# Optimization experiments

Hardware: AMD Instinct MI355X
Metric: run time of the kernel (lower is better)

## Reference

```python
import jax, jax.numpy as jnp
import numpy as np
import math

BASE_RES = 16; SCALE = 1.47; N_LEVELS = 16; FDIM = 2; MAX_SPLASH = 4
LOG2 = 17; HM = 1 << LOG2; SPLITS = [0.9375, 0.875]  # sorted descending as in module


def _build_cfg():
    res = [int(BASE_RES * SCALE ** i) for i in range(N_LEVELS)]
    ns = [0] * N_LEVELS
    for i in range(N_LEVELS):
        for j, s in enumerate(SPLITS):
            if i >= N_LEVELS * s:
                ns[i] = MAX_SPLASH // (2 ** j)
                break
    nidx = [min(r ** 3, HM) for r in res]
    nfeat = [nidx[i] * max(ns[i], 1) for i in range(N_LEVELS)]
    ngau = [nidx[i] * ns[i] for i in range(N_LEVELS)]
    fb = np.concatenate([[0], np.cumsum(nfeat)]).astype(np.int64)
    gb = np.concatenate([[0], np.cumsum(ngau)]).astype(np.int64)
    return res, ns, nidx, fb, gb

RES, NS, NIDX, FB, GB = _build_cfg()
OFFS = np.array([[(k >> 2) & 1, (k >> 1) & 1, k & 1] for k in range(8)], dtype=np.int32)
PRIMES = np.array([1, 2654435761, 805459861], dtype=np.uint32)
SQRT2PI = math.sqrt(2.0 * math.pi)


def _corners_coeffs(coords, res):
    # coords: (N,3) in [0,1). Returns corners (N,8,3) int32 and trilinear coeffs (N,8).
    x = jnp.clip(res * coords, 0.0, res - 1.001)
    pos = jnp.floor(x).astype(jnp.int32)
    xf = x - pos.astype(coords.dtype)
    offs = jnp.asarray(OFFS)
    corners = pos[:, None, :] + offs[None]
    w = jnp.where(offs[None].astype(bool), xf[:, None, :], 1.0 - xf[:, None, :])
    return corners, jnp.prod(w, axis=-1)


def _hash_index(corners, res):
    # linear index if grid fits in table, else xor-prime spatial hash (mod 2^17)
    if res ** 3 <= HM:
        return corners[..., 0] + corners[..., 1] * res + corners[..., 2] * (res * res)
    c = corners.astype(jnp.uint32)
    p = jnp.asarray(PRIMES)
    h = (c[..., 0] * p[0]) ^ (c[..., 1] * p[1]) ^ (c[..., 2] * p[2])
    return (h & jnp.uint32(HM - 1)).astype(jnp.int32)


def setup_inputs() -> dict:
    key = jax.random.key(0)
    k1, k2, k3, k4 = jax.random.split(key, 4)
    N = 262144
    coords = jax.random.uniform(k1, (N, 3), dtype=jnp.float32)
    feats = 0.01 * jax.random.normal(k2, (int(FB[-1]), FDIM), dtype=jnp.float32)
    # means: uniform in a ball of radius 0.25 centered at 0.5 (init_mean)
    G = int(GB[-1])
    pts = jax.random.normal(k3, (G, 3), dtype=jnp.float32)
    r = jnp.sqrt(jax.random.uniform(jax.random.fold_in(k3, 1), (G, 1), dtype=jnp.float32))
    means = pts / jnp.linalg.norm(pts, axis=1, keepdims=True) * r * 0.25 + 0.5
    # stds: N(0.125, 0.02) as in fixed_std=False branch
    stds = 0.125 + 0.02 * jax.random.normal(k4, (G, 1), dtype=jnp.float32)
    return {"coords": coords, "feats": feats, "means": means, "stds": stds}


def reference(coords, feats, means, stds):
    out_feats = []
    out_gmm = []
    for i in range(N_LEVELS):
        res = RES[i]; ns = NS[i]
        corners, coeffs = _corners_coeffs(coords, res)  # (N,8,3), (N,8)
        idx = _hash_index(corners, res)                 # (N,8)
        f = feats[int(FB[i]):int(FB[i + 1])].reshape(-1, max(ns, 1), FDIM)[idx]  # (N,8,S,F)
        if ns:
            m = means[int(GB[i]):int(GB[i + 1])].reshape(-1, ns, 3)[idx]   # (N,8,S,3)
            s = jnp.abs(stds[int(GB[i]):int(GB[i + 1])].reshape(-1, ns, 1)[idx])  # (N,8,S,1)
            diff = coords[:, None, None, :] - m
            sq = jnp.sum(diff * diff / (2.0 * s * s + 1e-7), axis=-1, keepdims=True)
            gw = jnp.exp(-sq) / (SQRT2PI * s + 1e-7)                        # Gaussian weights
            dw = jnp.sum(jnp.abs(diff / s) ** 2, axis=-1, keepdims=True)    # normalized sq dist
            out_feats.append(jnp.einsum('nc,ncsf->nf', coeffs, gw * f))
            out_gmm.append(jnp.einsum('nc,ncs->n', coeffs, (gw * dw)[..., 0]))
        else:
            out_feats.append(jnp.einsum('nc,ncf->nf', coeffs, f[:, :, 0, :]))
    return jnp.concatenate(out_feats, axis=-1), jnp.stack(out_gmm, axis=-1)
```

## Files before the change

kernel.cpp:

```cpp
#include <hip/hip_runtime.h>
#include <math.h>


#define HMASK 131071
typedef float vf4 __attribute__((ext_vector_type(4)));
typedef _Float16 h8 __attribute__((ext_vector_type(8)));
typedef _Float16 h2 __attribute__((ext_vector_type(2)));

__constant__ int c_fbh[10] = {180567,311639,442711,573783,704855,835927,
                              966999,1098071,1229143,1360215};

__device__ __forceinline__ void corner_setup(int res, float cx, float cy, float cz,
                                             int& px, int& py, int& pz,
                                             float& fx, float& fy, float& fz)
{
    const float hi = (float)((double)res - 1.001);
    float x = fminf(fmaxf((float)res * cx, 0.0f), hi);
    float y = fminf(fmaxf((float)res * cy, 0.0f), hi);
    float z = fminf(fmaxf((float)res * cz, 0.0f), hi);
    px = (int)x; py = (int)y; pz = (int)z;
    fx = x - (float)px; fy = y - (float)py; fz = z - (float)pz;
}

template<bool HASH>
__device__ __forceinline__ float2 plain_eval(
    int res, int fbase, float cx, float cy, float cz,
    const float* __restrict__ feats)
{
    int px, py, pz; float fx, fy, fz;
    corner_setup(res, cx, cy, cz, px, py, pz, fx, fy, fz);
    int   idxs[8];
    float ws[8];
#pragma unroll
    for (int k = 0; k < 8; ++k) {
        const int ox = (k >> 2) & 1, oy = (k >> 1) & 1, oz = k & 1;
        const int ix = px + ox, iy = py + oy, iz = pz + oz;
        ws[k] = (ox ? fx : 1.0f - fx) * (oy ? fy : 1.0f - fy) * (oz ? fz : 1.0f - fz);
        if (HASH) {
            unsigned h = (unsigned)ix ^ ((unsigned)iy * 2654435761u) ^ ((unsigned)iz * 805459861u);
            idxs[k] = (int)(h & HMASK);
        } else {
            idxs[k] = ix + iy * res + iz * res * res;
        }
    }
    float2 fv[8];
#pragma unroll
    for (int k = 0; k < 8; ++k)
        fv[k] = *(const float2*)(feats + (size_t)(fbase + idxs[k]) * 2);
    float a0 = 0.0f, a1 = 0.0f;
#pragma unroll
    for (int k = 0; k < 8; ++k) { a0 += ws[k] * fv[k].x; a1 += ws[k] * fv[k].y; }
    return make_float2(a0, a1);
}

__device__ __forceinline__ float2 plain_eval_h(
    int res, const h2* __restrict__ tab, float cx, float cy, float cz)
{
    int px, py, pz; float fx, fy, fz;
    corner_setup(res, cx, cy, cz, px, py, pz, fx, fy, fz);
    int   idxs[8];
    float ws[8];
#pragma unroll
    for (int k = 0; k < 8; ++k) {
        const int ox = (k >> 2) & 1, oy = (k >> 1) & 1, oz = k & 1;
        const int ix = px + ox, iy = py + oy, iz = pz + oz;
        ws[k] = (ox ? fx : 1.0f - fx) * (oy ? fy : 1.0f - fy) * (oz ? fz : 1.0f - fz);
        unsigned h = (unsigned)ix ^ ((unsigned)iy * 2654435761u) ^ ((unsigned)iz * 805459861u);
        idxs[k] = (int)(h & HMASK);
    }
    h2 fv[8];
#pragma unroll
    for (int k = 0; k < 8; ++k) fv[k] = tab[idxs[k]];
    float a0 = 0.0f, a1 = 0.0f;
#pragma unroll
    for (int k = 0; k < 8; ++k) { a0 += ws[k] * (float)fv[k][0]; a1 += ws[k] * (float)fv[k][1]; }
    return make_float2(a0, a1);
}

__device__ __forceinline__ void gauss_pre(float w, float dx, float dy, float dz,
                                          float i2s, float inrm, float is2,
                                          float f0, float f1,
                                          float& a0, float& a1, float& ag)
{
    const float d2 = dx*dx + dy*dy + dz*dz;
    const float sq = d2 * i2s;
    const float gw = __expf(-sq) * inrm;
    const float wg = w * gw;
    a0 += wg * f0;
    a1 += wg * f1;
    ag += wg * (d2 * is2);
}

__device__ __forceinline__ void splash14_part(
    int k0, float cx, float cy, float cz, float cox, float coy, float coz,
    const h8* __restrict__ slots, float& a0, float& a1, float& ag)
{
    int px, py, pz; float fx, fy, fz;
    corner_setup(3520, cx, cy, cz, px, py, pz, fx, fy, fz);
    a0 = 0.0f; a1 = 0.0f; ag = 0.0f;
#pragma unroll
    for (int kk = 0; kk < 4; ++kk) {
        const int k = k0 + kk;
        const int ox = (k >> 2) & 1, oy = (k >> 1) & 1, oz = k & 1;
        const int ix = px + ox, iy = py + oy, iz = pz + oz;
        const float w = (ox ? fx : 1.0f - fx) * (oy ? fy : 1.0f - fy) * (oz ? fz : 1.0f - fz);
        unsigned h = (unsigned)ix ^ ((unsigned)iy * 2654435761u) ^ ((unsigned)iz * 805459861u);
        const int idx = (int)(h & HMASK);
        const h8* sp = slots + (size_t)idx * 2;
        h8 A = sp[0], B = sp[1];
        gauss_pre(w, cox - (float)A[0], coy - (float)A[1], coz - (float)A[2],
                  (float)A[6], (float)B[0], (float)B[2], (float)B[4], (float)B[5], a0, a1, ag);
        gauss_pre(w, cox - (float)A[3], coy - (float)A[4], coz - (float)A[5],
                  (float)A[7], (float)B[1], (float)B[3], (float)B[6], (float)B[7], a0, a1, ag);
    }
}

__device__ __forceinline__ void splash15_part(
    int k0, float cx, float cy, float cz, float cox, float coy, float coz,
    const h8* __restrict__ slots, float& a0, float& a1, float& ag)
{
    int px, py, pz; float fx, fy, fz;
    corner_setup(5174, cx, cy, cz, px, py, pz, fx, fy, fz);
    a0 = 0.0f; a1 = 0.0f; ag = 0.0f;
#pragma unroll
    for (int kk = 0; kk < 2; ++kk) {
        const int k = k0 + kk;
        const int ox = (k >> 2) & 1, oy = (k >> 1) & 1, oz = k & 1;
        const int ix = px + ox, iy = py + oy, iz = pz + oz;
        const float w = (ox ? fx : 1.0f - fx) * (oy ? fy : 1.0f - fy) * (oz ? fz : 1.0f - fz);
        unsigned h = (unsigned)ix ^ ((unsigned)iy * 2654435761u) ^ ((unsigned)iz * 805459861u);
        const int idx = (int)(h & HMASK);
        const h8* sp = slots + (size_t)idx * 4;
        h8 A = sp[0], B = sp[1], C = sp[2], D = sp[3];
        gauss_pre(w, cox - (float)A[0], coy - (float)A[1], coz - (float)A[2],
                  (float)B[4], (float)C[0], (float)C[4], (float)D[0], (float)D[1], a0, a1, ag);
        gauss_pre(w, cox - (float)A[3], coy - (float)A[4], coz - (float)A[5],
                  (float)B[5], (float)C[1], (float)C[5], (float)D[2], (float)D[3], a0, a1, ag);
        gauss_pre(w, cox - (float)A[6], coy - (float)A[7], coz - (float)B[0],
                  (float)B[6], (float)C[2], (float)C[6], (float)D[4], (float)D[5], a0, a1, ag);
        gauss_pre(w, cox - (float)B[1], coy - (float)B[2], coz - (float)B[3],
                  (float)B[7], (float)C[3], (float)C[7], (float)D[6], (float)D[7], a0, a1, ag);
    }
}

template<int NS, int KN>
__device__ __forceinline__ void splash_direct_part(
    int k0, int res, int fbase, int gbase, float cx, float cy, float cz,
    const float* __restrict__ feats, const float* __restrict__ means,
    const float* __restrict__ stds, float& a0, float& a1, float& ag)
{
    int px, py, pz; float fx, fy, fz;
    corner_setup(res, cx, cy, cz, px, py, pz, fx, fy, fz);
    a0 = 0.0f; a1 = 0.0f; ag = 0.0f;
#pragma unroll
    for (int kk = 0; kk < KN; ++kk) {
        const int k = k0 + kk;
        const int ox = (k >> 2) & 1, oy = (k >> 1) & 1, oz = k & 1;
        const int ix = px + ox, iy = py + oy, iz = pz + oz;
        const float w = (ox ? fx : 1.0f - fx) * (oy ? fy : 1.0f - fy) * (oz ? fz : 1.0f - fz);
        unsigned h = (unsigned)ix ^ ((unsigned)iy * 2654435761u) ^ ((unsigned)iz * 805459861u);
        const int idx = (int)(h & HMASK);
        const int grow = gbase + idx * NS;
        const float* m = means + (size_t)grow * 3;
        const float* s = stds + grow;
        const float* f = feats + (size_t)(fbase + idx * NS) * 2;
#pragma unroll
        for (int si = 0; si < NS; ++si) {
            const float dx = cx - m[3*si], dy = cy - m[3*si+1], dz = cz - m[3*si+2];
            const float sva = fabsf(s[si]);
            const float d2 = dx*dx + dy*dy + dz*dz;
            const float s2 = sva * sva;
            const float sq = d2 / (2.0f * s2 + 1e-7f);
            const float gw = expf(-sq) / (2.5066282746310002f * sva + 1e-7f);
            const float wg = w * gw;
            a0 += wg * f[2*si];
            a1 += wg * f[2*si+1];
            ag += wg * (d2 / s2);
        }
    }
}

__global__ __launch_bounds__(256) void repack_kernel(
    const float* __restrict__ means, const float* __restrict__ stds,
    const float* __restrict__ feats, _Float16* __restrict__ ws)
{
    const int i = blockIdx.x * 256 + threadIdx.x;
    if (i < 1310720) {
        const int lvl = i >> 17;
        const int e   = i & 131071;
        const float2 f = *(const float2*)(feats + (size_t)(c_fbh[lvl] + e) * 2);
        h2 v; v[0] = (_Float16)f.x; v[1] = (_Float16)f.y;
        ((h2*)ws)[lvl * 131072 + e] = v;
    } else if (i < 1441792) {
        const int e = i - 1310720;
        const float2* m2 = (const float2*)(means + (size_t)e * 6);
        const float2 ma = m2[0], mb = m2[1], mc = m2[2];
        const float2 sv = *(const float2*)(stds + 2 * e);
        const float2* f2 = (const float2*)(feats + (size_t)(1491287 + 2 * e) * 2);
        const float2 fa = f2[0], fb = f2[1];
        const float s0 = fabsf(sv.x), s1 = fabsf(sv.y);
        h8 A, B;
        A[0] = (_Float16)(ma.x - 0.5f); A[1] = (_Float16)(ma.y - 0.5f); A[2] = (_Float16)(mb.x - 0.5f);
        A[3] = (_Float16)(mb.y - 0.5f); A[4] = (_Float16)(mc.x - 0.5f); A[5] = (_Float16)(mc.y - 0.5f);
        A[6] = (_Float16)(1.0f / (2.0f * s0 * s0 + 1e-7f));
        A[7] = (_Float16)(1.0f / (2.0f * s1 * s1 + 1e-7f));
        B[0] = (_Float16)(1.0f / (2.5066282746310002f * s0 + 1e-7f));
        B[1] = (_Float16)(1.0f / (2.5066282746310002f * s1 + 1e-7f));
        B[2] = (_Float16)(1.0f / (s0 * s0));
        B[3] = (_Float16)(1.0f / (s1 * s1));
        B[4] = (_Float16)fa.x; B[5] = (_Float16)fa.y; B[6] = (_Float16)fb.x; B[7] = (_Float16)fb.y;
        h8* dst = (h8*)(ws + 2621440) + (size_t)e * 2;
        dst[0] = A; dst[1] = B;
    } else {
        const int e = i - 1441792;
        const vf4* m4 = (const vf4*)(means + (size_t)(262144 + 4 * e) * 3);
        const vf4 u = m4[0], v = m4[1], w = m4[2];
        const vf4 s4 = *(const vf4*)(stds + 262144 + 4 * e);
        const float2* f2 = (const float2*)(feats + (size_t)(1753431 + 4 * e) * 2);
        const float2 fa = f2[0], fb = f2[1], fc = f2[2], fd = f2[3];
        h8 A, B, C, D;
        A[0] = (_Float16)(u.x - 0.5f); A[1] = (_Float16)(u.y - 0.5f); A[2] = (_Float16)(u.z - 0.5f);
        A[3] = (_Float16)(u.w - 0.5f); A[4] = (_Float16)(v.x - 0.5f); A[5] = (_Float16)(v.y - 0.5f);
        A[6] = (_Float16)(v.z - 0.5f); A[7] = (_Float16)(v.w - 0.5f);
        B[0] = (_Float16)(w.x - 0.5f); B[1] = (_Float16)(w.y - 0.5f);
        B[2] = (_Float16)(w.z - 0.5f); B[3] = (_Float16)(w.w - 0.5f);
        const float sv[4] = {fabsf(s4.x), fabsf(s4.y), fabsf(s4.z), fabsf(s4.w)};
#pragma unroll
        for (int t = 0; t < 4; ++t) {
            B[4 + t] = (_Float16)(1.0f / (2.0f * sv[t] * sv[t] + 1e-7f));
            C[t]     = (_Float16)(1.0f / (2.5066282746310002f * sv[t] + 1e-7f));
            C[4 + t] = (_Float16)(1.0f / (sv[t] * sv[t]));
        }
        D[0] = (_Float16)fa.x; D[1] = (_Float16)fa.y; D[2] = (_Float16)fb.x; D[3] = (_Float16)fb.y;
        D[4] = (_Float16)fc.x; D[5] = (_Float16)fc.y; D[6] = (_Float16)fd.x; D[7] = (_Float16)fd.y;
        h8* dst = (h8*)(ws + 4718592) + (size_t)e * 4;
        dst[0] = A; dst[1] = B; dst[2] = C; dst[3] = D;
    }
}

template<bool PACKED>
__global__ __launch_bounds__(256) void splash_enc(
    const float* __restrict__ coords, const float* __restrict__ feats,
    const float* __restrict__ means,  const float* __restrict__ stds,
    const _Float16* __restrict__ ws, float* __restrict__ out, int N)
{
    const int b = blockIdx.x;
    const int tid = threadIdx.x;
    const h2* tabs = (const h2*)ws;
    float* gmm = out + (size_t)N * 32;

    if (b < 1024) {
        const int n = b * 256 + tid;
        const float cx = coords[3*n+0], cy = coords[3*n+1], cz = coords[3*n+2];
        float2 acc[8];
        acc[0] = plain_eval<false>(16,       0, cx, cy, cz, feats);
        acc[1] = plain_eval<false>(23,    4096, cx, cy, cz, feats);
        acc[2] = plain_eval<false>(34,   16263, cx, cy, cz, feats);
        acc[3] = plain_eval<false>(50,   55567, cx, cy, cz, feats);
        if (PACKED) {
            acc[4] = plain_eval_h(74,  tabs + 0 * 131072, cx, cy, cz);
            acc[5] = plain_eval_h(109, tabs + 1 * 131072, cx, cy, cz);
            acc[6] = plain_eval_h(161, tabs + 2 * 131072, cx, cy, cz);
            acc[7] = plain_eval_h(237, tabs + 3 * 131072, cx, cy, cz);
        } else {
            acc[4] = plain_eval<true>(74,  180567, cx, cy, cz, feats);
            acc[5] = plain_eval<true>(109, 311639, cx, cy, cz, feats);
            acc[6] = plain_eval<true>(161, 442711, cx, cy, cz, feats);
            acc[7] = plain_eval<true>(237, 573783, cx, cy, cz, feats);
        }
        vf4* o = (vf4*)(out + (size_t)n * 32);
        o[0] = (vf4){acc[0].x, acc[0].y, acc[1].x, acc[1].y};
        o[1] = (vf4){acc[2].x, acc[2].y, acc[3].x, acc[3].y};
        o[2] = (vf4){acc[4].x, acc[4].y, acc[5].x, acc[5].y};
        o[3] = (vf4){acc[6].x, acc[6].y, acc[7].x, acc[7].y};
    } else if (b < 2048) {
        const int n = (b - 1024) * 256 + tid;
        const float cx = coords[3*n+0], cy = coords[3*n+1], cz = coords[3*n+2];
        float2 acc[6];
        if (PACKED) {
            acc[0] = plain_eval_h(348,  tabs + 4 * 131072, cx, cy, cz);
            acc[1] = plain_eval_h(512,  tabs + 5 * 131072, cx, cy, cz);
            acc[2] = plain_eval_h(753,  tabs + 6 * 131072, cx, cy, cz);
            acc[3] = plain_eval_h(1108, tabs + 7 * 131072, cx, cy, cz);
            acc[4] = plain_eval_h(1629, tabs + 8 * 131072, cx, cy, cz);
            acc[5] = plain_eval_h(2394, tabs + 9 * 131072, cx, cy, cz);
        } else {
            acc[0] = plain_eval<true>(348,   704855, cx, cy, cz, feats);
            acc[1] = plain_eval<true>(512,   835927, cx, cy, cz, feats);
            acc[2] = plain_eval<true>(753,   966999, cx, cy, cz, feats);
            acc[3] = plain_eval<true>(1108, 1098071, cx, cy, cz, feats);
            acc[4] = plain_eval<true>(1629, 1229143, cx, cy, cz, feats);
            acc[5] = plain_eval<true>(2394, 1360215, cx, cy, cz, feats);
        }
        vf4* o = (vf4*)(out + (size_t)n * 32);
        o[4] = (vf4){acc[0].x, acc[0].y, acc[1].x, acc[1].y};
        o[5] = (vf4){acc[2].x, acc[2].y, acc[3].x, acc[3].y};
        o[6] = (vf4){acc[4].x, acc[4].y, acc[5].x, acc[5].y};
    } else if (b < 4096) {
        const int t = (b - 2048) * 256 + tid;
        const int n = t >> 1, half = t & 1;
        const float cx = coords[3*n+0], cy = coords[3*n+1], cz = coords[3*n+2];
        float a0, a1, ag;
        if (PACKED) {
            splash14_part(half * 4, cx, cy, cz, cx - 0.5f, cy - 0.5f, cz - 0.5f,
                          (const h8*)(ws + 2621440), a0, a1, ag);
        } else {
            splash_direct_part<2,4>(half * 4, 3520, 1491287, 0, cx, cy, cz,
                                    feats, means, stds, a0, a1, ag);
        }
        a0 += __shfl_xor(a0, 1);
        a1 += __shfl_xor(a1, 1);
        ag += __shfl_xor(ag, 1);
        if (!half) {
            *(float2*)(out + (size_t)n * 32 + 28) = make_float2(a0, a1);
            gmm[2 * n] = ag;
        }
    } else {
        const int t = (b - 4096) * 256 + tid;
        const int n = t >> 2, q = t & 3;
        const float cx = coords[3*n+0], cy = coords[3*n+1], cz = coords[3*n+2];
        float a0, a1, ag;
        if (PACKED) {
            splash15_part(q * 2, cx, cy, cz, cx - 0.5f, cy - 0.5f, cz - 0.5f,
                          (const h8*)(ws + 4718592), a0, a1, ag);
        } else {
            splash_direct_part<4,2>(q * 2, 5174, 1753431, 262144, cx, cy, cz,
                                    feats, means, stds, a0, a1, ag);
        }
        a0 += __shfl_xor(a0, 1);
        a1 += __shfl_xor(a1, 1);
        ag += __shfl_xor(ag, 1);
        a0 += __shfl_xor(a0, 2);
        a1 += __shfl_xor(a1, 2);
        ag += __shfl_xor(ag, 2);
        if (q == 0) {
            *(float2*)(out + (size_t)n * 32 + 30) = make_float2(a0, a1);
            gmm[2 * n + 1] = ag;
        }
    }
}

extern "C" void kernel_launch(void* const* d_in, const int* in_sizes, int n_in,
                              void* d_out, int out_size, void* d_ws, size_t ws_size,
                              hipStream_t stream) {
    const float* coords = (const float*)d_in[0];
    const float* feats  = (const float*)d_in[1];
    const float* means  = (const float*)d_in[2];
    const float* stds   = (const float*)d_in[3];
    float* out = (float*)d_out;
    const int N = in_sizes[0] / 3;

    const bool packed = (ws_size >= 17825792);
    if (packed) {
        repack_kernel<<<6144, 256, 0, stream>>>(means, stds, feats, (_Float16*)d_ws);
        splash_enc<true><<<8192, 256, 0, stream>>>(coords, feats, means, stds,
                                                   (const _Float16*)d_ws, out, N);
    } else {
        splash_enc<false><<<8192, 256, 0, stream>>>(coords, feats, means, stds,
                                                    (const _Float16*)d_ws, out, N);
    }
}
```

Before: 239.5 us.

## Split per-point level work across more threads per point

```diff
diff --git a/kernel.cpp b/kernel.cpp
--- a/kernel.cpp
+++ b/kernel.cpp
@@ -9,12 +9,17 @@
 
 __constant__ int c_fbh[10] = {180567,311639,442711,573783,704855,835927,
                               966999,1098071,1229143,1360215};
+__constant__ int c_lres[4] = {16,23,34,50};
+__constant__ int c_lfb[4]  = {0,4096,16263,55567};
+__constant__ int c_h0res[4] = {74,109,161,237};
+__constant__ int c_p1resA[3] = {348,512,753};
+__constant__ int c_p1resB[3] = {1108,1629,2394};
 
 __device__ __forceinline__ void corner_setup(int res, float cx, float cy, float cz,
                                              int& px, int& py, int& pz,
                                              float& fx, float& fy, float& fz)
 {
-    const float hi = (float)((double)res - 1.001);
+    const float hi = (float)res - 1.001f;
     float x = fminf(fmaxf((float)res * cx, 0.0f), hi);
     float y = fminf(fmaxf((float)res * cy, 0.0f), hi);
     float z = fminf(fmaxf((float)res * cz, 0.0f), hi);
@@ -99,7 +104,7 @@
     corner_setup(3520, cx, cy, cz, px, py, pz, fx, fy, fz);
     a0 = 0.0f; a1 = 0.0f; ag = 0.0f;
 #pragma unroll
-    for (int kk = 0; kk < 4; ++kk) {
+    for (int kk = 0; kk < 2; ++kk) {
         const int k = k0 + kk;
         const int ox = (k >> 2) & 1, oy = (k >> 1) & 1, oz = k & 1;
         const int ix = px + ox, iy = py + oy, iz = pz + oz;
@@ -116,31 +121,27 @@
 }
 
 __device__ __forceinline__ void splash15_part(
-    int k0, float cx, float cy, float cz, float cox, float coy, float coz,
+    int k, float cx, float cy, float cz, float cox, float coy, float coz,
     const h8* __restrict__ slots, float& a0, float& a1, float& ag)
 {
     int px, py, pz; float fx, fy, fz;
     corner_setup(5174, cx, cy, cz, px, py, pz, fx, fy, fz);
     a0 = 0.0f; a1 = 0.0f; ag = 0.0f;
-#pragma unroll
-    for (int kk = 0; kk < 2; ++kk) {
-        const int k = k0 + kk;
-        const int ox = (k >> 2) & 1, oy = (k >> 1) & 1, oz = k & 1;
-        const int ix = px + ox, iy = py + oy, iz = pz + oz;
-        const float w = (ox ? fx : 1.0f - fx) * (oy ? fy : 1.0f - fy) * (oz ? fz : 1.0f - fz);
-        unsigned h = (unsigned)ix ^ ((unsigned)iy * 2654435761u) ^ ((unsigned)iz * 805459861u);
-        const int idx = (int)(h & HMASK);
-        const h8* sp = slots + (size_t)idx * 4;
-        h8 A = sp[0], B = sp[1], C = sp[2], D = sp[3];
-        gauss_pre(w, cox - (float)A[0], coy - (float)A[1], coz - (float)A[2],
-                  (float)B[4], (float)C[0], (float)C[4], (float)D[0], (float)D[1], a0, a1, ag);
-        gauss_pre(w, cox - (float)A[3], coy - (float)A[4], coz - (float)A[5],
-                  (float)B[5], (float)C[1], (float)C[5], (float)D[2], (float)D[3], a0, a1, ag);
-        gauss_pre(w, cox - (float)A[6], coy - (float)A[7], coz - (float)B[0],
-                  (float)B[6], (float)C[2], (float)C[6], (float)D[4], (float)D[5], a0, a1, ag);
-        gauss_pre(w, cox - (float)B[1], coy - (float)B[2], coz - (float)B[3],
-                  (float)B[7], (float)C[3], (float)C[7], (float)D[6], (float)D[7], a0, a1, ag);
-    }
+    const int ox = (k >> 2) & 1, oy = (k >> 1) & 1, oz = k & 1;
+    const int ix = px + ox, iy = py + oy, iz = pz + oz;
+    const float w = (ox ? fx : 1.0f - fx) * (oy ? fy : 1.0f - fy) * (oz ? fz : 1.0f - fz);
+    unsigned h = (unsigned)ix ^ ((unsigned)iy * 2654435761u) ^ ((unsigned)iz * 805459861u);
+    const int idx = (int)(h & HMASK);
+    const h8* sp = slots + (size_t)idx * 4;
+    h8 A = sp[0], B = sp[1], C = sp[2], D = sp[3];
+    gauss_pre(w, cox - (float)A[0], coy - (float)A[1], coz - (float)A[2],
+              (float)B[4], (float)C[0], (float)C[4], (float)D[0], (float)D[1], a0, a1, ag);
+    gauss_pre(w, cox - (float)A[3], coy - (float)A[4], coz - (float)A[5],
+              (float)B[5], (float)C[1], (float)C[5], (float)D[2], (float)D[3], a0, a1, ag);
+    gauss_pre(w, cox - (float)A[6], coy - (float)A[7], coz - (float)B[0],
+              (float)B[6], (float)C[2], (float)C[6], (float)D[4], (float)D[5], a0, a1, ag);
+    gauss_pre(w, cox - (float)B[1], coy - (float)B[2], coz - (float)B[3],
+              (float)B[7], (float)C[3], (float)C[7], (float)D[6], (float)D[7], a0, a1, ag);
 }
 
 template<int NS, int KN>
@@ -249,90 +250,64 @@
     const h2* tabs = (const h2*)ws;
     float* gmm = out + (size_t)N * 32;
 
-    if (b < 1024) {
-        const int n = b * 256 + tid;
+    if (b < 4096) {
+        const int t = b * 256 + tid;
+        const int n = t >> 2, q = t & 3;
         const float cx = coords[3*n+0], cy = coords[3*n+1], cz = coords[3*n+2];
-        float2 acc[8];
-        acc[0] = plain_eval<false>(16,       0, cx, cy, cz, feats);
-        acc[1] = plain_eval<false>(23,    4096, cx, cy, cz, feats);
-        acc[2] = plain_eval<false>(34,   16263, cx, cy, cz, feats);
-        acc[3] = plain_eval<false>(50,   55567, cx, cy, cz, feats);
+        float2 rlin = plain_eval<false>(c_lres[q], c_lfb[q], cx, cy, cz, feats);
+        float2 rhsh;
+        if (PACKED) rhsh = plain_eval_h(c_h0res[q], tabs + q * 131072, cx, cy, cz);
+        else        rhsh = plain_eval<true>(c_h0res[q], c_fbh[q], cx, cy, cz, feats);
+        *(float2*)(out + (size_t)n * 32 + 2 * q)     = rlin;
+        *(float2*)(out + (size_t)n * 32 + 8 + 2 * q) = rhsh;
+    } else if (b < 7168) {
+        const int t = (b - 4096) * 256 + tid;
+        const int n = (int)(((unsigned long long)(unsigned)t * 0xAAAAAAABull) >> 33);
+        const int q = t - 3 * n;
+        const float cx = coords[3*n+0], cy = coords[3*n+1], cz = coords[3*n+2];
+        float2 rA, rB;
         if (PACKED) {
-            acc[4] = plain_eval_h(74,  tabs + 0 * 131072, cx, cy, cz);
-            acc[5] = plain_eval_h(109, tabs + 1 * 131072, cx, cy, cz);
-            acc[6] = plain_eval_h(161, tabs + 2 * 131072, cx, cy, cz);
-            acc[7] = plain_eval_h(237, tabs + 3 * 131072, cx, cy, cz);
+            rA = plain_eval_h(c_p1resA[q], tabs + (4 + q) * 131072, cx, cy, cz);
+            rB = plain_eval_h(c_p1resB[q], tabs + (7 + q) * 131072, cx, cy, cz);
         } else {
-            acc[4] = plain_eval<true>(74,  180567, cx, cy, cz, feats);
-            acc[5] = plain_eval<true>(109, 311639, cx, cy, cz, feats);
-            acc[6] = plain_eval<true>(161, 442711, cx, cy, cz, feats);
-            acc[7] = plain_eval<true>(237, 573783, cx, cy, cz, feats);
-        }
-        vf4* o = (vf4*)(out + (size_t)n * 32);
-        o[0] = (vf4){acc[0].x, acc[0].y, acc[1].x, acc[1].y};
-        o[1] = (vf4){acc[2].x, acc[2].y, acc[3].x, acc[3].y};
-        o[2] = (vf4){acc[4].x, acc[4].y, acc[5].x, acc[5].y};
-        o[3] = (vf4){acc[6].x, acc[6].y, acc[7].x, acc[7].y};
-    } else if (b < 2048) {
-        const int n = (b - 1024) * 256 + tid;
-        const float cx = coords[3*n+0], cy = coords[3*n+1], cz = coords[3*n+2];
-        float2 acc[6];
-        if (PACKED) {
-            acc[0] = plain_eval_h(348,  tabs + 4 * 131072, cx, cy, cz);
-            acc[1] = plain_eval_h(512,  tabs + 5 * 131072, cx, cy, cz);
-            acc[2] = plain_eval_h(753,  tabs + 6 * 131072, cx, cy, cz);
-            acc[3] = plain_eval_h(1108, tabs + 7 * 131072, cx, cy, cz);
-            acc[4] = plain_eval_h(1629, tabs + 8 * 131072, cx, cy, cz);
-            acc[5] = plain_eval_h(2394, tabs + 9 * 131072, cx, cy, cz);
-        } else {
-            acc[0] = plain_eval<true>(348,   704855, cx, cy, cz, feats);
-            acc[1] = plain_eval<true>(512,   835927, cx, cy, cz, feats);
-            acc[2] = plain_eval<true>(753,   966999, cx, cy, cz, feats);
-            acc[3] = plain_eval<true>(1108, 1098071, cx, cy, cz, feats);
-            acc[4] = plain_eval<true>(1629, 1229143, cx, cy, cz, feats);
-            acc[5] = plain_eval<true>(2394, 1360215, cx, cy, cz, feats);
-        }
-        vf4* o = (vf4*)(out + (size_t)n * 32);
-        o[4] = (vf4){acc[0].x, acc[0].y, acc[1].x, acc[1].y};
-        o[5] = (vf4){acc[2].x, acc[2].y, acc[3].x, acc[3].y};
-        o[6] = (vf4){acc[4].x, acc[4].y, acc[5].x, acc[5].y};
-    } else if (b < 4096) {
-        const int t = (b - 2048) * 256 + tid;
-        const int n = t >> 1, half = t & 1;
-        const float cx = coords[3*n+0], cy = coords[3*n+1], cz = coords[3*n+2];
-        float a0, a1, ag;
-        if (PACKED) {
-            splash14_part(half * 4, cx, cy, cz, cx - 0.5f, cy - 0.5f, cz - 0.5f,
-                          (const h8*)(ws + 2621440), a0, a1, ag);
-        } else {
-            splash_direct_part<2,4>(half * 4, 3520, 1491287, 0, cx, cy, cz,
-                                    feats, means, stds, a0, a1, ag);
-        }
-        a0 += __shfl_xor(a0, 1);
-        a1 += __shfl_xor(a1, 1);
-        ag += __shfl_xor(ag, 1);
-        if (!half) {
-            *(float2*)(out + (size_t)n * 32 + 28) = make_float2(a0, a1);
-            gmm[2 * n] = ag;
-        }
-    } else {
-        const int t = (b - 4096) * 256 + tid;
+            rA = plain_eval<true>(c_p1resA[q], c_fbh[4 + q], cx, cy, cz, feats);
+            rB = plain_eval<true>(c_p1resB[q], c_fbh[7 + q], cx, cy, cz, feats);
+        }
+        *(float2*)(out + (size_t)n * 32 + 16 + 2 * q) = rA;
+        *(float2*)(out + (size_t)n * 32 + 22 + 2 * q) = rB;
+    } else if (b < 11264) {
+        const int t = (b - 7168) * 256 + tid;
         const int n = t >> 2, q = t & 3;
         const float cx = coords[3*n+0], cy = coords[3*n+1], cz = coords[3*n+2];
         float a0, a1, ag;
         if (PACKED) {
-            splash15_part(q * 2, cx, cy, cz, cx - 0.5f, cy - 0.5f, cz - 0.5f,
+            splash14_part(q * 2, cx, cy, cz, cx - 0.5f, cy - 0.5f, cz - 0.5f,
+                          (const h8*)(ws + 2621440), a0, a1, ag);
+        } else {
+            splash_direct_part<2,2>(q * 2, 3520, 1491287, 0, cx, cy, cz,
+                                    feats, means, stds, a0, a1, ag);
+        }
+        a0 += __shfl_xor(a0, 1); a1 += __shfl_xor(a1, 1); ag += __shfl_xor(ag, 1);
+        a0 += __shfl_xor(a0, 2); a1 += __shfl_xor(a1, 2); ag += __shfl_xor(ag, 2);
+        if (q == 0) {
+            *(float2*)(out + (size_t)n * 32 + 28) = make_float2(a0, a1);
+            gmm[2 * n] = ag;
+        }
+    } else {
+        const int t = (b - 11264) * 256 + tid;
+        const int n = t >> 3, q = t & 7;
+        const float cx = coords[3*n+0], cy = coords[3*n+1], cz = coords[3*n+2];
+        float a0, a1, ag;
+        if (PACKED) {
+            splash15_part(q, cx, cy, cz, cx - 0.5f, cy - 0.5f, cz - 0.5f,
                           (const h8*)(ws + 4718592), a0, a1, ag);
         } else {
-            splash_direct_part<4,2>(q * 2, 5174, 1753431, 262144, cx, cy, cz,
+            splash_direct_part<4,1>(q, 5174, 1753431, 262144, cx, cy, cz,
                                     feats, means, stds, a0, a1, ag);
         }
-        a0 += __shfl_xor(a0, 1);
-        a1 += __shfl_xor(a1, 1);
-        ag += __shfl_xor(ag, 1);
-        a0 += __shfl_xor(a0, 2);
-        a1 += __shfl_xor(a1, 2);
-        ag += __shfl_xor(ag, 2);
+        a0 += __shfl_xor(a0, 1); a1 += __shfl_xor(a1, 1); ag += __shfl_xor(ag, 1);
+        a0 += __shfl_xor(a0, 2); a1 += __shfl_xor(a1, 2); ag += __shfl_xor(ag, 2);
+        a0 += __shfl_xor(a0, 4); a1 += __shfl_xor(a1, 4); ag += __shfl_xor(ag, 4);
         if (q == 0) {
             *(float2*)(out + (size_t)n * 32 + 30) = make_float2(a0, a1);
             gmm[2 * n + 1] = ag;
@@ -353,10 +328,10 @@
     const bool packed = (ws_size >= 17825792);
     if (packed) {
         repack_kernel<<<6144, 256, 0, stream>>>(means, stds, feats, (_Float16*)d_ws);
-        splash_enc<true><<<8192, 256, 0, stream>>>(coords, feats, means, stds,
-                                                   (const _Float16*)d_ws, out, N);
+        splash_enc<true><<<19456, 256, 0, stream>>>(coords, feats, means, stds,
+                                                    (const _Float16*)d_ws, out, N);
     } else {
-        splash_enc<false><<<8192, 256, 0, stream>>>(coords, feats, means, stds,
-                                                    (const _Float16*)d_ws, out, N);
-    }
-}
+        splash_enc<false><<<19456, 256, 0, stream>>>(coords, feats, means, stds,
+                                                     (const _Float16*)d_ws, out, N);
+    }
+}
```

Result: faster. 233.3 us (-2.6%).
